# Kernel optimization log

Hardware: AMD Instinct MI355X
Metric: run time of the kernel (lower is better)

The kernel has to match this reference:

```python
import jax, jax.numpy as jnp
import numpy as np

N, D = 6144, 128
NUM_CLASSES, NUM_BATCHES = 20, 5
MIN_T, MAX_T = 0.1, 1.0
TEMP_BATCH = 0.5  # fixed per-batch-key temperature set in __init__
EPS = 1e-8        # F.cosine_similarity eps


def _class_weights(labels, n):
    c = jnp.bincount(labels, length=n).astype(jnp.float32)
    w = 1.0 / c
    return w / w.sum()


def setup_inputs() -> dict:
    key = jax.random.key(0)
    k1, k2, k3 = jax.random.split(key, 3)
    x = jax.random.normal(k1, (N, D), dtype=jnp.float32)
    targets = jax.random.randint(k2, (N,), 0, NUM_CLASSES)
    batch0 = jax.random.randint(k3, (N,), 0, NUM_BATCHES)
    return {
        "input": x,
        "temperature": jnp.float32(0.25),
        "weight_target": _class_weights(targets, NUM_CLASSES),
        "weight_batch0": _class_weights(batch0, NUM_BATCHES),
        "targets": targets,
        "batch0": batch0,
    }


def _snn_losses(S, pos_mask, neg_mask):
    # S: [N,N] exp-similarities; masks include/exclude self consistently with torch code
    diag = jnp.diagonal(S)
    pos_sum = jnp.einsum('ij,ij->i', S, pos_mask.astype(S.dtype)) - diag  # self is in pos_mask
    neg_sum = jnp.einsum('ij,ij->i', S, neg_mask.astype(S.dtype))
    cnt_pos = pos_mask.sum(axis=1)  # includes self
    cnt_neg = neg_mask.sum(axis=1)
    valid = (cnt_pos >= 2) & (cnt_neg >= 1)
    pos_safe = jnp.where(valid, pos_sum, 1.0)
    neg_safe = jnp.where(valid, neg_sum, 1.0)
    loss_i = -jnp.log(pos_safe / (pos_safe + neg_safe))
    return loss_i, valid


def _weighted_class_sum(loss_i, valid, labels, weights, num_segments):
    lsum = jax.ops.segment_sum(jnp.where(valid, loss_i, 0.0), labels, num_segments=num_segments)
    cnt = jax.ops.segment_sum(valid.astype(jnp.float32), labels, num_segments=num_segments)
    mean = lsum / jnp.maximum(cnt, 1.0)
    return jnp.sum(jnp.where(cnt > 0, mean * weights, 0.0))


def reference(input, temperature, weight_target, weight_batch0, targets, batch0):
    t = jnp.clip(temperature, MIN_T, MAX_T)
    norms = jnp.maximum(jnp.linalg.norm(input, axis=1, keepdims=True), EPS)
    xn = input / norms
    sim = xn @ xn.T  # [N, N] cosine similarity

    same_t = targets[:, None] == targets[None, :]

    # ----- target (cell-type) SNN loss -----
    S_t = jnp.exp(sim / t)
    loss_i, valid = _snn_losses(S_t, same_t, ~same_t)
    loss_target = _weighted_class_sum(loss_i, valid, targets, weight_target, NUM_CLASSES)

    # ----- batch-effect loss (one batch key), reciprocal of -log -----
    S_b = jnp.exp(sim / TEMP_BATCH)
    same_b = batch0[:, None] == batch0[None, :]
    pos_mask = same_t & same_b
    neg_mask = same_t & (~same_b)
    loss_bi, valid_b = _snn_losses(S_b, pos_mask, neg_mask)
    loss_bi = jnp.where(valid_b, 1.0 / jnp.where(valid_b, loss_bi, 1.0), 0.0)
    loss_batch = _weighted_class_sum(loss_bi, valid_b, batch0, weight_batch0, NUM_BATCHES)
    # single batch key -> mean over batch keys is just loss_batch

    return 0.9 * loss_target + 0.1 * loss_batch
```

## Files before the change

kernel.cpp:

```cpp
#include <hip/hip_runtime.h>
#include <hip/hip_bf16.h>
#include <math.h>

#define NN 6144
#define DD 128
#define NCLS 20
#define NBATCH 5
#define NB 48
#define NPAIR (NB * (NB + 1) / 2)

typedef float f32x4 __attribute__((ext_vector_type(4)));
typedef short bf16x8 __attribute__((ext_vector_type(8)));

#define SOFF (NN * DD / 2)
#define AOFF (SOFF + 4 * NN)
#define COFF (AOFF + 50)

__global__ __launch_bounds__(256) void k_prep(const float* __restrict__ x,
                                              float* __restrict__ ws) {
    const int t = threadIdx.x;
    if (blockIdx.x < 24) {
        float4 z = {0.f, 0.f, 0.f, 0.f};
        *(float4*)(ws + SOFF + blockIdx.x * 1024 + t * 4) = z;
    } else if (blockIdx.x == 24) {
        if (t < 51) ws[AOFF + t] = 0.0f;
    }
    const int lane = t & 63;
    const int row = blockIdx.x * 4 + (t >> 6);
    float2 v = *(const float2*)(x + row * DD + 2 * lane);
    float s = v.x * v.x + v.y * v.y;
#pragma unroll
    for (int m = 1; m < 64; m <<= 1) s += __shfl_xor(s, m, 64);
    float rinv = 1.0f / fmaxf(sqrtf(s), 1e-8f);
    __hip_bfloat16 h0 = __float2bfloat16(v.x * rinv);
    __hip_bfloat16 h1 = __float2bfloat16(v.y * rinv);
    ushort2 u;
    u.x = *(ushort*)&h0;
    u.y = *(ushort*)&h1;
    ushort* xnb = (ushort*)ws;
    *(ushort2*)(xnb + row * DD + 2 * lane) = u;
}

#define RED16(v)                                                      \
    {                                                                 \
        float s0 = up3 ? v[0] : v[2], k0 = up3 ? v[2] : v[0];         \
        float s1 = up3 ? v[1] : v[3], k1 = up3 ? v[3] : v[1];         \
        v[0] = k0 + __shfl_xor(s0, 8, 64);                            \
        v[1] = k1 + __shfl_xor(s1, 8, 64);                            \
        float s2 = up2 ? v[0] : v[1], k2 = up2 ? v[1] : v[0];         \
        v[0] = k2 + __shfl_xor(s2, 4, 64);                            \
        v[0] += __shfl_xor(v[0], 2, 64);                              \
        v[0] += __shfl_xor(v[0], 1, 64);                              \
    }

#define RED4(v)                                                       \
    {                                                                 \
        float s0 = q1 ? v[0] : v[2], k0 = q1 ? v[2] : v[0];           \
        float s1 = q1 ? v[1] : v[3], k1 = q1 ? v[3] : v[1];           \
        v[0] = k0 + __shfl_xor(s0, 32, 64);                           \
        v[1] = k1 + __shfl_xor(s1, 32, 64);                           \
        float s2 = q0 ? v[0] : v[1], k2 = q0 ? v[1] : v[0];           \
        v[0] = k2 + __shfl_xor(s2, 16, 64);                           \
    }

__global__ __launch_bounds__(256) void k_main(const float* __restrict__ temp,
                                              const int* __restrict__ tg,
                                              const int* __restrict__ bt,
                                              float* __restrict__ ws) {
    __shared__ __align__(16) char smem[36864];
    __shared__ int tgA[128], btA[128], tgB[128], btB[128];

    ushort (*tA)[72] = (ushort(*)[72])smem;
    ushort (*tB)[72] = (ushort(*)[72])(smem + 18432);
    float* sRowF = (float*)smem;
    float* sColF = (float*)(smem + 4096);

    const ushort* xnb = (const ushort*)ws;
    float* PT = ws + SOFF;
    float* TT = PT + NN;
    float* PB = PT + 2 * NN;
    float* TB = PT + 3 * NN;

    int bi = 0, rem = blockIdx.x;
    while (rem >= NB - bi) { rem -= NB - bi; ++bi; }
    const int bj = bi + rem;
    const int I = bi * 128, J = bj * 128;
    const bool isDiag = (bi == bj);

    const int t = threadIdx.x;
    const int w = t >> 6;
    const int lane = t & 63;
    const int tx16 = lane & 15;
    const int quad = lane >> 4;
    const int rowBase = (w >> 1) * 64;
    const int colBase = (w & 1) * 64;

    const float tc = fminf(fmaxf(temp[0], 0.1f), 1.0f);
    const float c1 = 1.4426950408889634f / tc;
    const float c2 = 2.8853900817779268f;

    if (t < 128) { tgA[t] = tg[I + t]; btA[t] = bt[I + t]; }
    else { int u2 = t - 128; tgB[u2] = tg[J + u2]; btB[u2] = bt[J + u2]; }

    f32x4 acc[4][4];
#pragma unroll
    for (int mt = 0; mt < 4; ++mt)
#pragma unroll
        for (int nt = 0; nt < 4; ++nt) acc[mt][nt] = (f32x4){0.f, 0.f, 0.f, 0.f};

    for (int kc = 0; kc < 2; ++kc) {
        if (kc) __syncthreads();
        {
            const int r0 = t >> 3, ch = t & 7;
            const ushort* gA = xnb + (I + r0) * DD + kc * 64 + ch * 8;
            const ushort* gB = xnb + (J + r0) * DD + kc * 64 + ch * 8;
#pragma unroll
            for (int it = 0; it < 4; ++it) {
                *(float4*)&tA[r0 + 32 * it][ch * 8] = *(const float4*)(gA + 32 * it * DD);
                *(float4*)&tB[r0 + 32 * it][ch * 8] = *(const float4*)(gB + 32 * it * DD);
            }
        }
        __syncthreads();
#pragma unroll
        for (int ks = 0; ks < 2; ++ks) {
            bf16x8 a[4], b[4];
            const int ko = ks * 32 + quad * 8;
#pragma unroll
            for (int mt = 0; mt < 4; ++mt)
                a[mt] = *(const bf16x8*)&tA[rowBase + 16 * mt + tx16][ko];
#pragma unroll
            for (int nt = 0; nt < 4; ++nt)
                b[nt] = *(const bf16x8*)&tB[colBase + 16 * nt + tx16][ko];
#pragma unroll
            for (int mt = 0; mt < 4; ++mt)
#pragma unroll
                for (int nt = 0; nt < 4; ++nt)
                    acc[mt][nt] = __builtin_amdgcn_mfma_f32_16x16x32_bf16(
                        a[mt], b[nt], acc[mt][nt], 0, 0, 0);
        }
    }

    __syncthreads();

    float cPT[4] = {0}, cTT[4] = {0}, cPB[4] = {0}, cTB[4] = {0};
    int tjv[4], bjv[4];
#pragma unroll
    for (int nt = 0; nt < 4; ++nt) {
        int jl = colBase + 16 * nt + tx16;
        tjv[nt] = tgB[jl];
        bjv[nt] = btB[jl];
    }
    const bool up3 = (tx16 >> 3) & 1;
    const bool up2 = (tx16 >> 2) & 1;
    const int pOwn = tx16 >> 2;

#pragma unroll
    for (int mt = 0; mt < 4; ++mt) {
        float rPT[4] = {0}, rTT[4] = {0}, rPB[4] = {0}, rTB[4] = {0};
        int til[4], bil[4];
#pragma unroll
        for (int p = 0; p < 4; ++p) {
            int il = rowBase + 16 * mt + 4 * quad + p;
            til[p] = tgA[il];
            bil[p] = btA[il];
        }
        if (isDiag) {
#pragma unroll
            for (int nt = 0; nt < 4; ++nt) {
                const int jl = colBase + 16 * nt + tx16;
#pragma unroll
                for (int p = 0; p < 4; ++p) {
                    const int il = rowBase + 16 * mt + 4 * quad + p;
                    float s = acc[mt][nt][p];
                    float et = __builtin_amdgcn_exp2f(c1 * s);
                    float eb = __builtin_amdgcn_exp2f(c2 * s);
                    bool nd = (il != jl);
                    bool st = (til[p] == tjv[nt]) && nd;
                    bool sb = (bil[p] == bjv[nt]);
                    rTT[p] += nd ? et : 0.f;
                    rPT[p] += st ? et : 0.f;
                    rTB[p] += st ? eb : 0.f;
                    rPB[p] += (st && sb) ? eb : 0.f;
                }
            }
        } else {
#pragma unroll
            for (int nt = 0; nt < 4; ++nt) {
#pragma unroll
                for (int p = 0; p < 4; ++p) {
                    float s = acc[mt][nt][p];
                    float et = __builtin_amdgcn_exp2f(c1 * s);
                    float eb = __builtin_amdgcn_exp2f(c2 * s);
                    bool st = (til[p] == tjv[nt]);
                    bool sb = (bil[p] == bjv[nt]);
                    float etp = st ? et : 0.f;
                    float ebp = st ? eb : 0.f;
                    float ebb = (st && sb) ? eb : 0.f;
                    rTT[p] += et;
                    rPT[p] += etp;
                    rTB[p] += ebp;
                    rPB[p] += ebb;
                    cTT[nt] += et;
                    cPT[nt] += etp;
                    cTB[nt] += ebp;
                    cPB[nt] += ebb;
                }
            }
        }
        RED16(rPT);
        RED16(rTT);
        RED16(rPB);
        RED16(rTB);
        if ((tx16 & 3) == 0) {
            int il = rowBase + 16 * mt + 4 * quad + pOwn;
            int rep = (w & 1) * 512;
            sRowF[rep + 0 * 128 + il] = rPT[0];
            sRowF[rep + 1 * 128 + il] = rTT[0];
            sRowF[rep + 2 * 128 + il] = rPB[0];
            sRowF[rep + 3 * 128 + il] = rTB[0];
        }
    }
    if (!isDiag) {
        const bool q1 = (quad >> 1) & 1;
        const bool q0 = quad & 1;
        RED4(cPT);
        RED4(cTT);
        RED4(cPB);
        RED4(cTB);
        int cl = colBase + 16 * quad + tx16;
        int rep = (w >> 1) * 512;
        sColF[rep + 0 * 128 + cl] = cPT[0];
        sColF[rep + 1 * 128 + cl] = cTT[0];
        sColF[rep + 2 * 128 + cl] = cPB[0];
        sColF[rep + 3 * 128 + cl] = cTB[0];
    }

    __syncthreads();
    if (t < 128) {
        int gi = I + t;
        atomicAdd(&PT[gi], sRowF[0 * 128 + t] + sRowF[512 + 0 * 128 + t]);
        atomicAdd(&TT[gi], sRowF[1 * 128 + t] + sRowF[512 + 1 * 128 + t]);
        atomicAdd(&PB[gi], sRowF[2 * 128 + t] + sRowF[512 + 2 * 128 + t]);
        atomicAdd(&TB[gi], sRowF[3 * 128 + t] + sRowF[512 + 3 * 128 + t]);
    } else if (!isDiag) {
        int u2 = t - 128;
        int gj = J + u2;
        atomicAdd(&PT[gj], sColF[0 * 128 + u2] + sColF[512 + 0 * 128 + u2]);
        atomicAdd(&TT[gj], sColF[1 * 128 + u2] + sColF[512 + 1 * 128 + u2]);
        atomicAdd(&PB[gj], sColF[2 * 128 + u2] + sColF[512 + 2 * 128 + u2]);
        atomicAdd(&TB[gj], sColF[3 * 128 + u2] + sColF[512 + 3 * 128 + u2]);
    }
}

__global__ __launch_bounds__(256) void k_fin(const int* __restrict__ tg,
                                             const int* __restrict__ bt,
                                             const float* __restrict__ wt,
                                             const float* __restrict__ wb,
                                             float* __restrict__ ws,
                                             float* __restrict__ out) {
    __shared__ int hh[NCLS + NCLS * NBATCH];
    __shared__ float ph[4][52];
    __shared__ int lastFlag;
    const int t = threadIdx.x;
    const int wv = t >> 6;
    if (t < NCLS + NCLS * NBATCH) hh[t] = 0;
    if (t < 52 * 4) ((float*)ph)[t] = 0.0f;
    __syncthreads();
    for (int i = t; i < NN; i += 256) {
        int c = tg[i], b = bt[i];
        atomicAdd(&hh[c], 1);
        atomicAdd(&hh[NCLS + c * NBATCH + b], 1);
    }
    __syncthreads();
    const float* PT = ws + SOFF;
    const float* TT = PT + NN;
    const float* PB = PT + 2 * NN;
    const float* TB = PT + 3 * NN;
    {
        const int i = blockIdx.x * 256 + t;
        float pt = PT[i], tt = TT[i], pb = PB[i], tb = TB[i];
        int ti = tg[i], bi = bt[i];
        int cp = hh[ti];
        int cpb = hh[NCLS + ti * NBATCH + bi];
        if (cp >= 2 && (NN - cp) >= 1) {
            float loss = logf(tt / pt);
            atomicAdd(&ph[wv][ti], loss);
            atomicAdd(&ph[wv][20 + ti], 1.0f);
        }
        if (cpb >= 2 && (cp - cpb) >= 1) {
            float lb = logf(tb / pb);
            atomicAdd(&ph[wv][40 + bi], 1.0f / lb);
            atomicAdd(&ph[wv][45 + bi], 1.0f);
        }
    }
    __syncthreads();
    if (t < 50) {
        float s = ph[0][t] + ph[1][t] + ph[2][t] + ph[3][t];
        atomicAdd(&ws[AOFF + t], s);
    }
    __syncthreads();
    if (t == 0) {
        __threadfence();
        lastFlag = (atomicAdd((int*)(ws + COFF), 1) == 23) ? 1 : 0;
    }
    __syncthreads();
    if (lastFlag) {
        __threadfence();
        if (t < 64) {
            const float* acc = ws + AOFF;
            float term = 0.0f;
            if (t < NCLS) {
                float cnt = acc[NCLS + t];
                if (cnt > 0.f) term = 0.9f * (acc[t] / cnt) * wt[t];
            } else if (t >= 32 && t < 32 + NBATCH) {
                int b = t - 32;
                float cnt = acc[2 * NCLS + NBATCH + b];
                if (cnt > 0.f) term = 0.1f * (acc[2 * NCLS + b] / cnt) * wb[b];
            }
#pragma unroll
            for (int m = 1; m < 64; m <<= 1) term += __shfl_xor(term, m, 64);
            if (t == 0) out[0] = term;
        }
    }
}

extern "C" void kernel_launch(void* const* d_in, const int* in_sizes, int n_in,
                              void* d_out, int out_size, void* d_ws, size_t ws_size,
                              hipStream_t stream) {
    const float* x    = (const float*)d_in[0];
    const float* temp = (const float*)d_in[1];
    const float* wt   = (const float*)d_in[2];
    const float* wb   = (const float*)d_in[3];
    const int*   tg   = (const int*)d_in[4];
    const int*   bt   = (const int*)d_in[5];
    float* out = (float*)d_out;
    float* ws = (float*)d_ws;

    k_prep<<<NN / 4, 256, 0, stream>>>(x, ws);
    k_main<<<NPAIR, 256, 0, stream>>>(temp, tg, bt, ws);
    k_fin<<<24, 256, 0, stream>>>(tg, bt, wt, wb, ws, out);
}
```

Measured before the change: 100.2 us.

## Replace global atomics with per-block-column strips and subtract diagonal analytically

Each tile now writes its row and column partial sums as float4 into a per-strip buffer instead of doing atomicAdds on global accumulators, and the final kernel sums the 48 strips per row. The diagonal special-case branch is removed: tiles on the diagonal use the generic path, and the self term is subtracted in the final kernel from the recomputed bf16 self-dot. This drops the zeroing of accumulators in prep and the atomic contention, and adds a launch-bounds occupancy hint. In exchange, the final pass reads 48 strips per row, and the self-term subtraction may differ slightly from the MFMA-computed diagonal value.

After: 203.1 us. +102.6%, slower.

```diff
diff --git a/kernel.cpp b/kernel.cpp
--- a/kernel.cpp
+++ b/kernel.cpp
@@ -13,18 +13,15 @@
 typedef short bf16x8 __attribute__((ext_vector_type(8)));
 
 #define SOFF (NN * DD / 2)
-#define AOFF (SOFF + 4 * NN)
+#define DOFF SOFF
+#define STOFF (DOFF + NN)
+#define AOFF (STOFF + NB * NN * 4)
 #define COFF (AOFF + 50)
 
 __global__ __launch_bounds__(256) void k_prep(const float* __restrict__ x,
                                               float* __restrict__ ws) {
     const int t = threadIdx.x;
-    if (blockIdx.x < 24) {
-        float4 z = {0.f, 0.f, 0.f, 0.f};
-        *(float4*)(ws + SOFF + blockIdx.x * 1024 + t * 4) = z;
-    } else if (blockIdx.x == 24) {
-        if (t < 51) ws[AOFF + t] = 0.0f;
-    }
+    if (blockIdx.x == 24 && t < 51) ws[AOFF + t] = 0.0f;
     const int lane = t & 63;
     const int row = blockIdx.x * 4 + (t >> 6);
     float2 v = *(const float2*)(x + row * DD + 2 * lane);
@@ -34,6 +31,11 @@
     float rinv = 1.0f / fmaxf(sqrtf(s), 1e-8f);
     __hip_bfloat16 h0 = __float2bfloat16(v.x * rinv);
     __hip_bfloat16 h1 = __float2bfloat16(v.y * rinv);
+    float f0 = __bfloat162float(h0), f1 = __bfloat162float(h1);
+    float s2 = f0 * f0 + f1 * f1;
+#pragma unroll
+    for (int m = 1; m < 64; m <<= 1) s2 += __shfl_xor(s2, m, 64);
+    if (lane == 0) ws[DOFF + row] = s2;
     ushort2 u;
     u.x = *(ushort*)&h0;
     u.y = *(ushort*)&h1;
@@ -63,10 +65,10 @@
         v[0] = k2 + __shfl_xor(s2, 16, 64);                           \
     }
 
-__global__ __launch_bounds__(256) void k_main(const float* __restrict__ temp,
-                                              const int* __restrict__ tg,
-                                              const int* __restrict__ bt,
-                                              float* __restrict__ ws) {
+__global__ __launch_bounds__(256, 4) void k_main(const float* __restrict__ temp,
+                                                 const int* __restrict__ tg,
+                                                 const int* __restrict__ bt,
+                                                 float* __restrict__ ws) {
     __shared__ __align__(16) char smem[36864];
     __shared__ int tgA[128], btA[128], tgB[128], btB[128];
 
@@ -76,10 +78,7 @@
     float* sColF = (float*)(smem + 4096);
 
     const ushort* xnb = (const ushort*)ws;
-    float* PT = ws + SOFF;
-    float* TT = PT + NN;
-    float* PB = PT + 2 * NN;
-    float* TB = PT + 3 * NN;
+    float* strips = ws + STOFF;
 
     int bi = 0, rem = blockIdx.x;
     while (rem >= NB - bi) { rem -= NB - bi; ++bi; }
@@ -164,47 +163,26 @@
             til[p] = tgA[il];
             bil[p] = btA[il];
         }
-        if (isDiag) {
-#pragma unroll
-            for (int nt = 0; nt < 4; ++nt) {
-                const int jl = colBase + 16 * nt + tx16;
-#pragma unroll
-                for (int p = 0; p < 4; ++p) {
-                    const int il = rowBase + 16 * mt + 4 * quad + p;
-                    float s = acc[mt][nt][p];
-                    float et = __builtin_amdgcn_exp2f(c1 * s);
-                    float eb = __builtin_amdgcn_exp2f(c2 * s);
-                    bool nd = (il != jl);
-                    bool st = (til[p] == tjv[nt]) && nd;
-                    bool sb = (bil[p] == bjv[nt]);
-                    rTT[p] += nd ? et : 0.f;
-                    rPT[p] += st ? et : 0.f;
-                    rTB[p] += st ? eb : 0.f;
-                    rPB[p] += (st && sb) ? eb : 0.f;
-                }
-            }
-        } else {
-#pragma unroll
-            for (int nt = 0; nt < 4; ++nt) {
-#pragma unroll
-                for (int p = 0; p < 4; ++p) {
-                    float s = acc[mt][nt][p];
-                    float et = __builtin_amdgcn_exp2f(c1 * s);
-                    float eb = __builtin_amdgcn_exp2f(c2 * s);
-                    bool st = (til[p] == tjv[nt]);
-                    bool sb = (bil[p] == bjv[nt]);
-                    float etp = st ? et : 0.f;
-                    float ebp = st ? eb : 0.f;
-                    float ebb = (st && sb) ? eb : 0.f;
-                    rTT[p] += et;
-                    rPT[p] += etp;
-                    rTB[p] += ebp;
-                    rPB[p] += ebb;
-                    cTT[nt] += et;
-                    cPT[nt] += etp;
-                    cTB[nt] += ebp;
-                    cPB[nt] += ebb;
-                }
+#pragma unroll
+        for (int nt = 0; nt < 4; ++nt) {
+#pragma unroll
+            for (int p = 0; p < 4; ++p) {
+                float s = acc[mt][nt][p];
+                float et = __builtin_amdgcn_exp2f(c1 * s);
+                float eb = __builtin_amdgcn_exp2f(c2 * s);
+                bool st = (til[p] == tjv[nt]);
+                bool sb = (bil[p] == bjv[nt]);
+                float etp = st ? et : 0.f;
+                float ebp = st ? eb : 0.f;
+                float ebb = (st && sb) ? eb : 0.f;
+                rTT[p] += et;
+                rPT[p] += etp;
+                rTB[p] += ebp;
+                rPB[p] += ebb;
+                cTT[nt] += et;
+                cPT[nt] += etp;
+                cTB[nt] += ebp;
+                cPB[nt] += ebb;
             }
         }
         RED16(rPT);
@@ -237,22 +215,25 @@
 
     __syncthreads();
     if (t < 128) {
-        int gi = I + t;
-        atomicAdd(&PT[gi], sRowF[0 * 128 + t] + sRowF[512 + 0 * 128 + t]);
-        atomicAdd(&TT[gi], sRowF[1 * 128 + t] + sRowF[512 + 1 * 128 + t]);
-        atomicAdd(&PB[gi], sRowF[2 * 128 + t] + sRowF[512 + 2 * 128 + t]);
-        atomicAdd(&TB[gi], sRowF[3 * 128 + t] + sRowF[512 + 3 * 128 + t]);
+        float4 v;
+        v.x = sRowF[0 * 128 + t] + sRowF[512 + 0 * 128 + t];
+        v.y = sRowF[1 * 128 + t] + sRowF[512 + 1 * 128 + t];
+        v.z = sRowF[2 * 128 + t] + sRowF[512 + 2 * 128 + t];
+        v.w = sRowF[3 * 128 + t] + sRowF[512 + 3 * 128 + t];
+        *(float4*)&strips[(size_t)(bj * NN + I + t) * 4] = v;
     } else if (!isDiag) {
         int u2 = t - 128;
-        int gj = J + u2;
-        atomicAdd(&PT[gj], sColF[0 * 128 + u2] + sColF[512 + 0 * 128 + u2]);
-        atomicAdd(&TT[gj], sColF[1 * 128 + u2] + sColF[512 + 1 * 128 + u2]);
-        atomicAdd(&PB[gj], sColF[2 * 128 + u2] + sColF[512 + 2 * 128 + u2]);
-        atomicAdd(&TB[gj], sColF[3 * 128 + u2] + sColF[512 + 3 * 128 + u2]);
+        float4 v;
+        v.x = sColF[0 * 128 + u2] + sColF[512 + 0 * 128 + u2];
+        v.y = sColF[1 * 128 + u2] + sColF[512 + 1 * 128 + u2];
+        v.z = sColF[2 * 128 + u2] + sColF[512 + 2 * 128 + u2];
+        v.w = sColF[3 * 128 + u2] + sColF[512 + 3 * 128 + u2];
+        *(float4*)&strips[(size_t)(bi * NN + J + u2) * 4] = v;
     }
 }
 
-__global__ __launch_bounds__(256) void k_fin(const int* __restrict__ tg,
+__global__ __launch_bounds__(256) void k_fin(const float* __restrict__ temp,
+                                             const int* __restrict__ tg,
                                              const int* __restrict__ bt,
                                              const float* __restrict__ wt,
                                              const float* __restrict__ wb,
@@ -272,13 +253,28 @@
         atomicAdd(&hh[NCLS + c * NBATCH + b], 1);
     }
     __syncthreads();
-    const float* PT = ws + SOFF;
-    const float* TT = PT + NN;
-    const float* PB = PT + 2 * NN;
-    const float* TB = PT + 3 * NN;
+    const float* strips = ws + STOFF;
+    const float tc = fminf(fmaxf(temp[0], 0.1f), 1.0f);
+    const float c1 = 1.4426950408889634f / tc;
+    const float c2 = 2.8853900817779268f;
     {
         const int i = blockIdx.x * 256 + t;
-        float pt = PT[i], tt = TT[i], pb = PB[i], tb = TB[i];
+        float pt = 0.f, tt = 0.f, pb = 0.f, tb = 0.f;
+#pragma unroll 8
+        for (int s = 0; s < NB; ++s) {
+            float4 v = *(const float4*)&strips[(size_t)(s * NN + i) * 4];
+            pt += v.x;
+            tt += v.y;
+            pb += v.z;
+            tb += v.w;
+        }
+        float s2 = ws[DOFF + i];
+        float e1 = __builtin_amdgcn_exp2f(c1 * s2);
+        float e2 = __builtin_amdgcn_exp2f(c2 * s2);
+        pt -= e1;
+        tt -= e1;
+        pb -= e2;
+        tb -= e2;
         int ti = tg[i], bi = bt[i];
         int cp = hh[ti];
         int cpb = hh[NCLS + ti * NBATCH + bi];
@@ -338,5 +334,5 @@
 
     k_prep<<<NN / 4, 256, 0, stream>>>(x, ws);
     k_main<<<NPAIR, 256, 0, stream>>>(temp, tg, bt, ws);
-    k_fin<<<24, 256, 0, stream>>>(tg, bt, wt, wb, ws, out);
+    k_fin<<<24, 256, 0, stream>>>(temp, tg, bt, wt, wb, ws, out);
 }
```
